# Performance work log

Hardware: AMD Instinct MI355X
Metric: run time of the kernel (lower is better)

Reference implementation:

```python
import jax, jax.numpy as jnp
import numpy as np

B, CIN, COUT, H, W = 16, 96, 96, 96, 96
K = 3   # hidden_kernels (conv), odd -> same padding
A = 3   # attn_kernels, odd -> stride-1 unfold preserves H*W positions


def _conv(x, w, p):
    # NCHW conv with symmetric padding p, stride 1, no bias
    return jax.lax.conv_general_dilated(
        x, w, window_strides=(1, 1), padding=[(p, p), (p, p)],
        dimension_numbers=("NCHW", "OIHW", "NCHW"))


def _unfold_nonoverlap(y, a):
    # torch nn.Unfold(a, stride=a): [B,C,H,W] -> [B, C*a*a, L], channel-major (c,kh,kw)
    b, c, h, w = y.shape
    hb, wb = h // a, w // a
    y = y.reshape(b, c, hb, a, wb, a).transpose(0, 1, 3, 5, 2, 4)
    return y.reshape(b, c * a * a, hb * wb)


def _unfold_stride1(y, a):
    # torch nn.Unfold(a, padding=a//2): [B,C,H,W] -> [B, C*a*a, H*W]
    b, c, h, w = y.shape
    p = a // 2
    yp = jnp.pad(y, ((0, 0), (0, 0), (p, p), (p, p)))
    # small fixed a*a loop (9 shifts), channel-major (c,kh,kw) ordering
    patches = jnp.stack([yp[:, :, i:i + h, j:j + w]
                         for i in range(a) for j in range(a)], axis=2)
    return patches.reshape(b, c * a * a, h * w)


def setup_inputs() -> dict:
    key = jax.random.key(0)
    kx, k1, k2, k3 = jax.random.split(key, 4)
    x = jax.random.normal(kx, (B, CIN, H, W), dtype=jnp.float32)
    W1 = jax.random.normal(k1, (COUT, CIN, K, K), dtype=jnp.float32) * 0.05
    W2 = jax.random.normal(k2, (COUT, CIN, K, K), dtype=jnp.float32) * 0.05
    W3 = jax.random.normal(k3, (COUT, CIN, K, K), dtype=jnp.float32) * 0.05
    return {"x": x, "W1": W1, "W2": W2, "W3": W3}


def reference(x, W1, W2, W3):
    a, c, p = A, COUT, K // 2
    b = x.shape[0]
    y1 = _unfold_nonoverlap(_conv(x, W1, p), a)   # [B, C*a^2, L]
    y2 = _unfold_nonoverlap(_conv(x, W2, p), a)   # [B, C*a^2, L]
    L = y1.shape[-1]
    y1 = y1.reshape(b, c, a * a, L).transpose(0, 2, 1, 3)  # [B, a^2, C, L]
    y2 = y2.reshape(b, c, a * a, L).transpose(0, 2, 3, 1)  # [B, a^2, L, C]
    attn = jnp.einsum("bkcl,bkld->bkcd", y1, y2)           # [B, a^2, C, C]
    # torch: transpose(1,3).flatten(2) -> [B, C, C*a^2], then scale + softmax(dim=2)
    attn = attn.transpose(0, 3, 2, 1).reshape(b, c, c * a * a)
    attn = jax.nn.softmax(attn / np.float32(np.sqrt(c * a * a)), axis=2)
    v = _unfold_stride1(_conv(x, W3, p), a)        # [B, C*a^2, H*W]
    out = jnp.einsum("bcm,bml->bcl", attn, v)      # [B, C, H*W]
    return out.reshape(b, c, H, W)
```

## Files before the change

kernel.cpp:

```cpp
#include <hip/hip_runtime.h>
#include <math.h>
#include <stdint.h>

constexpr int BB  = 16;
constexpr int CH  = 96;
constexpr int HH  = 96;
constexpr int WW  = 96;
constexpr int HWI = HH * WW;
constexpr int CHW = CH * HWI;
constexpr int IMG = BB * CHW;
constexpr int ATT = BB * CH * CH * 9;
constexpr int WPK = 27 * 6 * 64 * 8;

typedef short short8 __attribute__((ext_vector_type(8)));
typedef float floatx4 __attribute__((ext_vector_type(4)));

__device__ __forceinline__ ushort f2bf(float f) {
  union { float f; unsigned u; } v; v.f = f;
  unsigned r = (v.u + 0x7fffu + ((v.u >> 16) & 1u)) >> 16;
  return (ushort)r;
}
__device__ __forceinline__ float bf2f(ushort h) {
  union { float f; unsigned u; } v; v.u = ((unsigned)h) << 16;
  return v.f;
}
__device__ __forceinline__ uint packhl(float v) {
  const ushort h = f2bf(v);
  const ushort l = f2bf(v - bf2f(h));
  return (uint)h | ((uint)l << 16);
}

__device__ __forceinline__ void gl_lds_b128(const void* g, void* s) {
  auto gp = (const __attribute__((address_space(1))) void*)(uintptr_t)g;
  auto sp = (__attribute__((address_space(3))) void*)(uintptr_t)s;
  __builtin_amdgcn_global_load_lds(gp, sp, 16, 0, 0);
}

__global__ __launch_bounds__(256) void xcast(
    const float* __restrict__ X, ushort* __restrict__ Xn)
{
  const int b  = blockIdx.y;
  const int p0 = blockIdx.x * 256;
  const int tid = threadIdx.x;
  __shared__ ushort T[256 * 104];

  const float* xb = X + (size_t)b * CHW + p0;
#pragma unroll 8
  for (int c = 0; c < 96; c += 2) {
    const ushort h0 = f2bf(xb[(size_t)c * HWI + tid]);
    const ushort h1 = f2bf(xb[(size_t)(c + 1) * HWI + tid]);
    *(uint*)(&T[tid * 104 + c]) = (uint)h0 | ((uint)h1 << 16);
  }
  __syncthreads();

  ushort* ob = Xn + (size_t)b * CHW + (size_t)p0 * 96;
#pragma unroll
  for (int it = 0; it < 12; ++it) {
    const int idx = it * 256 + tid;
    const int pix = (idx * 2731) >> 15;
    const int c8  = idx - pix * 12;
    *(short8*)(ob + pix * 96 + c8 * 8) = *(const short8*)(&T[pix * 104 + c8 * 8]);
  }
}

__global__ __launch_bounds__(256) void prepack(
    const float* __restrict__ src, ushort* __restrict__ dst)
{
  const int g = blockIdx.y;
  const int p = blockIdx.x * 256 + threadIdx.x;
  const float* s = src + (size_t)g * WPK;
  ushort* d = dst + (size_t)g * WPK;
  const int j    = p & 7;
  const int lane = (p >> 3) & 63;
  const int rest = p >> 9;
  const int mt = rest % 6;
  const int kc = rest / 6;
  const int m  = mt * 16 + (lane & 15);
  const int k  = kc * 32 + (lane >> 4) * 8 + j;
  const int ci = k % 96;
  const int o  = k / 96;
  d[p] = f2bf(s[m * 864 + ci * 9 + o]);
}

template<int OUTM>
__global__ __launch_bounds__(256, 1) void conv_nb(
    const ushort* __restrict__ Xn,
    const ushort* __restrict__ Wpk,
    void* __restrict__ Yv, int wbstride)
{
  const int b    = blockIdx.y;
  const int tile = blockIdx.x;
  const int ty0  = (tile / 6) * 12;
  const int tx0  = (tile % 6) * 16;
  const int tid  = threadIdx.x;
  const int lane = tid & 63;
  const int w    = tid >> 6;
  const int nc   = lane & 15;
  const int q    = lane >> 4;

  __shared__ __attribute__((aligned(16))) ushort Xs[252 * 104];
  __shared__ __attribute__((aligned(16))) ushort Ws[9 * 3072];

  const ushort* wp = Wpk + (size_t)b * wbstride;

  for (int i = 0; i < 14; ++i) {
    const int pp = w + 4 * i;
    if (pp < 54)
      gl_lds_b128(wp + (size_t)pp * 512 + lane * 8,
                  (ushort*)Ws + __builtin_amdgcn_readfirstlane(pp * 512));
  }

  const ushort* xb = Xn + (size_t)b * CHW;
  for (int it = 0; it < 12; ++it) {
    const int idx = it * 256 + tid;
    if (idx < 3024) {
      const int pix = (idx * 2731) >> 15;
      const int c8  = idx - pix * 12;
      const int ly  = (pix * 57) >> 10;
      const int lx  = pix - ly * 18;
      const int gy  = ty0 - 1 + ly, gx = tx0 - 1 + lx;
      short8 v = {0, 0, 0, 0, 0, 0, 0, 0};
      if (((unsigned)gy < 96u) & ((unsigned)gx < 96u))
        v = *(const short8*)(xb + ((size_t)gy * WW + gx) * 96 + c8 * 8);
      *(short8*)(&Xs[pix * 104 + c8 * 8]) = v;
    }
  }
  __syncthreads();

  floatx4 acc[6][3];
#pragma unroll
  for (int mt = 0; mt < 6; ++mt)
#pragma unroll
    for (int t = 0; t < 3; ++t)
#pragma unroll
      for (int r = 0; r < 4; ++r) acc[mt][t][r] = 0.f;

  for (int g = 0; g < 3; ++g) {
    if (g) {
      __syncthreads();
      for (int i = 0; i < 14; ++i) {
        const int pp = w + 4 * i;
        if (pp < 54)
          gl_lds_b128(wp + (size_t)(g * 54 + pp) * 512 + lane * 8,
                      (ushort*)Ws + __builtin_amdgcn_readfirstlane(pp * 512));
      }
      __syncthreads();
    }

#pragma unroll
    for (int oo = 0; oo < 3; ++oo) {
#pragma unroll
      for (int cc = 0; cc < 3; ++cc) {
        const int kcL = oo * 3 + cc;
        const int pc  = nc + oo;
        const int cib = cc * 32 + q * 8;

        short8 bfr[3];
#pragma unroll
        for (int t = 0; t < 3; ++t) {
          const int pix = (3 * w + t + g) * 18 + pc;
          bfr[t] = *(const short8*)(&Xs[pix * 104 + cib]);
        }

        const ushort* ap = (const ushort*)Ws + kcL * 3072 + lane * 8;
#pragma unroll
        for (int mt = 0; mt < 6; ++mt) {
          const short8 af = *(const short8*)(ap + mt * 512);
#pragma unroll
          for (int t = 0; t < 3; ++t)
            acc[mt][t] = __builtin_amdgcn_mfma_f32_16x16x32_bf16(
                af, bfr[t], acc[mt][t], 0, 0, 0);
        }
      }
    }
  }

#pragma unroll
  for (int mt = 0; mt < 6; ++mt)
#pragma unroll
    for (int t = 0; t < 3; ++t) {
      const int yy = ty0 + 3 * w + t;
      const int xx = tx0 + nc;
#pragma unroll
      for (int r = 0; r < 4; ++r) {
        const int co = mt * 16 + q * 4 + r;
        if constexpr (OUTM == 0) {
          ((uint*)Yv + (size_t)b * CHW)[(size_t)co * HWI + yy * WW + xx] =
              packhl(acc[mt][t][r]);
        } else if constexpr (OUTM == 1) {
          ((ushort*)Yv + (size_t)b * CHW)[((size_t)yy * WW + xx) * 96 + co] =
              f2bf(acc[mt][t][r]);
        } else {
          ((float*)Yv + (size_t)b * CHW)[(size_t)co * HWI + yy * WW + xx] =
              acc[mt][t][r];
        }
      }
    }
}

__global__ __launch_bounds__(256) void attn_mfma(
    const uint* __restrict__ Y1, const uint* __restrict__ Y2,
    float* __restrict__ P0, float* __restrict__ P1,
    float* __restrict__ P2, float* __restrict__ P3)
{
  const int bi = blockIdx.x;
  const int b  = bi / 36;
  const int r9 = bi % 36;
  const int k  = r9 >> 2;
  const int qd = r9 & 3;
  const int kh = k / 3, kw = k % 3;
  const int tid  = threadIdx.x;
  const int lane = tid & 63;
  const int wv   = tid >> 6;

  __shared__ ushort Ah[96 * 72], Al[96 * 72], Bh[96 * 72], Bl[96 * 72];

  const uint* y1b = Y1 + (size_t)b * CHW;
  const uint* y2b = Y2 + (size_t)b * CHW;

  const int mg2 = wv >> 1;
  const int ng2 = wv & 1;
  const int cn = lane & 15;
  const int q  = lane >> 4;

  floatx4 acc[3][3];
#pragma unroll
  for (int i = 0; i < 3; ++i)
#pragma unroll
    for (int j = 0; j < 3; ++j)
#pragma unroll
      for (int r = 0; r < 4; ++r) acc[i][j][r] = 0.f;

  const int sj = tid & 31;
  const int sg = tid >> 5;
  const int scol = 3 * sj + kw;

  for (int ss = 0; ss < 4; ++ss) {
    const int s = qd * 4 + ss;
    __syncthreads();
#pragma unroll
    for (int cg = 0; cg < 12; ++cg) {
      const int c = cg * 8 + sg;
      const int cbase = c * 72;
#pragma unroll
      for (int ii = 0; ii < 2; ++ii) {
        const int row = 3 * (s * 2 + ii) + kh;
        const int p   = ii * 32 + sj;
        const size_t goff = (size_t)c * HWI + row * WW + scol;
        const uint u1 = y1b[goff];
        const uint u2 = y2b[goff];
        Ah[cbase + p] = (ushort)(u1 & 0xffffu);
        Al[cbase + p] = (ushort)(u1 >> 16);
        Bh[cbase + p] = (ushort)(u2 & 0xffffu);
        Bl[cbase + p] = (ushort)(u2 >> 16);
      }
    }
    __syncthreads();

#pragma unroll
    for (int kc = 0; kc < 2; ++kc) {
      short8 ah[3], al[3], bh[3], bl[3];
#pragma unroll
      for (int t = 0; t < 3; ++t) {
        const int offA = (mg2 * 48 + t * 16 + cn) * 72 + kc * 32 + q * 8;
        ah[t] = *(const short8*)(&Ah[offA]);
        al[t] = *(const short8*)(&Al[offA]);
        const int offB = (ng2 * 48 + t * 16 + cn) * 72 + kc * 32 + q * 8;
        bh[t] = *(const short8*)(&Bh[offB]);
        bl[t] = *(const short8*)(&Bl[offB]);
      }
#pragma unroll
      for (int i = 0; i < 3; ++i)
#pragma unroll
        for (int j = 0; j < 3; ++j) {
          acc[i][j] = __builtin_amdgcn_mfma_f32_16x16x32_bf16(
              ah[i], bh[j], acc[i][j], 0, 0, 0);
          acc[i][j] = __builtin_amdgcn_mfma_f32_16x16x32_bf16(
              ah[i], bl[j], acc[i][j], 0, 0, 0);
          acc[i][j] = __builtin_amdgcn_mfma_f32_16x16x32_bf16(
              al[i], bh[j], acc[i][j], 0, 0, 0);
        }
    }
  }

  float* P = (qd == 0) ? P0 : (qd == 1) ? P1 : (qd == 2) ? P2 : P3;
#pragma unroll
  for (int i = 0; i < 3; ++i)
#pragma unroll
    for (int j = 0; j < 3; ++j)
#pragma unroll
      for (int r = 0; r < 4; ++r) {
        const int c = mg2 * 48 + i * 16 + q * 4 + r;
        const int d = ng2 * 48 + j * 16 + cn;
        P[((size_t)(b * CH + d) * CH + c) * 9 + k] = acc[i][j][r];
      }
}

__global__ __launch_bounds__(256) void softmax_k(
    const float* __restrict__ P0, const float* __restrict__ P1,
    const float* __restrict__ P2, const float* __restrict__ P3,
    float* __restrict__ attnW)
{
  const int bd = blockIdx.x;
  const size_t base = (size_t)bd * 864;
  float* dst = attnW + base;
  const float rs = 0.0340216824f;
  const int tid = threadIdx.x;

  const size_t i0 = base + tid;
  float v0 = P0[i0] + P1[i0] + P2[i0] + P3[i0];
  float v1 = P0[i0 + 256] + P1[i0 + 256] + P2[i0 + 256] + P3[i0 + 256];
  float v2 = P0[i0 + 512] + P1[i0 + 512] + P2[i0 + 512] + P3[i0 + 512];
  float v3 = (tid < 96)
      ? (P0[i0 + 768] + P1[i0 + 768] + P2[i0 + 768] + P3[i0 + 768])
      : -3.0e38f;

  float mx = fmaxf(fmaxf(v0, v1), fmaxf(v2, v3));

  __shared__ float red[256];
  red[tid] = mx;
  __syncthreads();
#pragma unroll
  for (int s = 128; s > 0; s >>= 1) {
    if (tid < s) red[tid] = fmaxf(red[tid], red[tid + s]);
    __syncthreads();
  }
  mx = red[0];
  __syncthreads();

  const float e0 = expf((v0 - mx) * rs);
  const float e1 = expf((v1 - mx) * rs);
  const float e2 = expf((v2 - mx) * rs);
  const float e3 = (tid < 96) ? expf((v3 - mx) * rs) : 0.f;

  red[tid] = e0 + e1 + e2 + e3;
  __syncthreads();
#pragma unroll
  for (int s = 128; s > 0; s >>= 1) {
    if (tid < s) red[tid] += red[tid + s];
    __syncthreads();
  }
  const float inv = 1.f / red[0];

  dst[tid]       = e0 * inv;
  dst[tid + 256] = e1 * inv;
  dst[tid + 512] = e2 * inv;
  if (tid < 96) dst[tid + 768] = e3 * inv;
}

extern "C" void kernel_launch(void* const* d_in, const int* in_sizes, int n_in,
                              void* d_out, int out_size, void* d_ws, size_t ws_size,
                              hipStream_t stream)
{
  const float* x  = (const float*)d_in[0];
  const float* W1 = (const float*)d_in[1];
  const float* W2 = (const float*)d_in[2];
  const float* W3 = (const float*)d_in[3];

  float* ws    = (float*)d_ws;
  uint*  Y1    = (uint*)ws;
  uint*  Y2    = Y1 + (size_t)IMG;
  float* attnT = (float*)(Y2 + (size_t)IMG);
  float* attnW = attnT + ATT;
  ushort* pk   = (ushort*)(attnW + ATT);
  ushort* pkW1 = pk;
  ushort* pkW2 = pk + WPK;
  ushort* pkW3 = pk + 2 * (size_t)WPK;
  ushort* pkAW = pk + 3 * (size_t)WPK;
  ushort* Xn   = pkAW + 16 * (size_t)WPK;
  float* Pd2   = (float*)d_out;
  float* Pd3   = Pd2 + ATT;
  ushort* Y3n  = (ushort*)Y1;

  const dim3 cgrid(48, BB);

  xcast    <<<dim3(36, BB), 256, 0, stream>>>(x, Xn);

  prepack  <<<dim3(324, 1),  256, 0, stream>>>(W1, pkW1);
  prepack  <<<dim3(324, 1),  256, 0, stream>>>(W2, pkW2);
  prepack  <<<dim3(324, 1),  256, 0, stream>>>(W3, pkW3);

  conv_nb<0><<<cgrid, 256, 0, stream>>>(Xn, pkW1, Y1, 0);
  conv_nb<0><<<cgrid, 256, 0, stream>>>(Xn, pkW2, Y2, 0);

  attn_mfma<<<BB * 9 * 4, 256, 0, stream>>>(Y1, Y2, attnT, attnW, Pd2, Pd3);
  softmax_k<<<BB * CH, 256, 0, stream>>>(attnT, attnW, Pd2, Pd3, attnW);

  prepack  <<<dim3(324, BB), 256, 0, stream>>>(attnW, pkAW);

  conv_nb<1><<<cgrid, 256, 0, stream>>>(Xn, pkW3, Y3n, 0);
  conv_nb<2><<<cgrid, 256, 0, stream>>>(Y3n, pkAW, d_out, WPK);
}
```

Before: 391.5 us.

## Write conv1/conv2 outputs in unfolded block-major layout for vectorized attention loads

The conv epilogue for the Y1/Y2 outputs now writes directly into an unfold-ordered layout [B, 9, C, 1024], indexed by the position within each 3x3 block and the block index. The attention kernel can then load contiguous 16-byte chunks per channel instead of strided scalar gathers with stride 3, and it writes split hi/lo halves to LDS as packed uint2 stores. This trades scattered (less coalesced) stores in the conv epilogue for fully coalesced vector loads and fewer LDS writes in the attention kernel.

```diff
diff --git a/kernel.cpp b/kernel.cpp
--- a/kernel.cpp
+++ b/kernel.cpp
@@ -185,7 +185,11 @@
       for (int r = 0; r < 4; ++r) {
         const int co = mt * 16 + q * 4 + r;
         if constexpr (OUTM == 0) {
-          ((uint*)Yv + (size_t)b * CHW)[(size_t)co * HWI + yy * WW + xx] =
+          const int cx = xx / 3;
+          const int kw = xx - 3 * cx;
+          const int kk = t * 3 + kw;
+          const int cp = (ty0 / 3 + w) * 32 + cx;
+          ((uint*)Yv)[(((size_t)b * 9 + kk) * CH + co) * 1024 + cp] =
               packhl(acc[mt][t][r]);
         } else if constexpr (OUTM == 1) {
           ((ushort*)Yv + (size_t)b * CHW)[((size_t)yy * WW + xx) * 96 + co] =
@@ -208,15 +212,14 @@
   const int r9 = bi % 36;
   const int k  = r9 >> 2;
   const int qd = r9 & 3;
-  const int kh = k / 3, kw = k % 3;
   const int tid  = threadIdx.x;
   const int lane = tid & 63;
   const int wv   = tid >> 6;
 
   __shared__ ushort Ah[96 * 72], Al[96 * 72], Bh[96 * 72], Bl[96 * 72];
 
-  const uint* y1b = Y1 + (size_t)b * CHW;
-  const uint* y2b = Y2 + (size_t)b * CHW;
+  const uint* y1b = Y1 + ((size_t)(b * 9 + k) * CH) * 1024;
+  const uint* y2b = Y2 + ((size_t)(b * 9 + k) * CH) * 1024;
 
   const int mg2 = wv >> 1;
   const int ng2 = wv & 1;
@@ -231,29 +234,32 @@
 #pragma unroll
       for (int r = 0; r < 4; ++r) acc[i][j][r] = 0.f;
 
-  const int sj = tid & 31;
-  const int sg = tid >> 5;
-  const int scol = 3 * sj + kw;
+  const int sj4  = tid & 15;
+  const int sg16 = tid >> 4;
 
   for (int ss = 0; ss < 4; ++ss) {
     const int s = qd * 4 + ss;
     __syncthreads();
 #pragma unroll
-    for (int cg = 0; cg < 12; ++cg) {
-      const int c = cg * 8 + sg;
-      const int cbase = c * 72;
-#pragma unroll
-      for (int ii = 0; ii < 2; ++ii) {
-        const int row = 3 * (s * 2 + ii) + kh;
-        const int p   = ii * 32 + sj;
-        const size_t goff = (size_t)c * HWI + row * WW + scol;
-        const uint u1 = y1b[goff];
-        const uint u2 = y2b[goff];
-        Ah[cbase + p] = (ushort)(u1 & 0xffffu);
-        Al[cbase + p] = (ushort)(u1 >> 16);
-        Bh[cbase + p] = (ushort)(u2 & 0xffffu);
-        Bl[cbase + p] = (ushort)(u2 >> 16);
-      }
+    for (int cg = 0; cg < 6; ++cg) {
+      const int c = cg * 16 + sg16;
+      const size_t goff = (size_t)c * 1024 + s * 64 + sj4 * 4;
+      const uint4 u1 = *(const uint4*)(y1b + goff);
+      const uint4 u2 = *(const uint4*)(y2b + goff);
+      const int lbase = c * 72 + sj4 * 4;
+      uint2 w;
+      w.x = (u1.x & 0xffffu) | (u1.y << 16);
+      w.y = (u1.z & 0xffffu) | (u1.w << 16);
+      *(uint2*)(&Ah[lbase]) = w;
+      w.x = (u1.x >> 16) | (u1.y & 0xffff0000u);
+      w.y = (u1.z >> 16) | (u1.w & 0xffff0000u);
+      *(uint2*)(&Al[lbase]) = w;
+      w.x = (u2.x & 0xffffu) | (u2.y << 16);
+      w.y = (u2.z & 0xffffu) | (u2.w << 16);
+      *(uint2*)(&Bh[lbase]) = w;
+      w.x = (u2.x >> 16) | (u2.y & 0xffff0000u);
+      w.y = (u2.z >> 16) | (u2.w & 0xffff0000u);
+      *(uint2*)(&Bl[lbase]) = w;
     }
     __syncthreads();
 
```

Measured after the change: 385.2 us. No clear change (-1.6%).
